# Kernel tuning notes

Hardware: AMD Instinct MI355X
Metric: run time of the kernel (lower is better)

## Reference

```python
import jax, jax.numpy as jnp
import numpy as np

N = 100_000          # nodes
E = 3_200_000        # edges (avg degree 32)
USER_SIZE = 80_000
CAT_SIZE = 5_000
USER_DIM = 8
CAT_DIM = 4
IN_CH = 8
OUT_CH = 16
HID = 16


def setup_inputs() -> dict:
    key = jax.random.key(0)
    ks = jax.random.split(key, 24)
    # features: [N,3] int; col0 = id (user id if type==0 else category id), col1 = known flag in {0,1}, col2 = type in {0,1}
    typ = jax.random.randint(ks[0], (N,), 0, 2)
    uid = jax.random.randint(ks[1], (N,), 0, USER_SIZE)
    cid = jax.random.randint(ks[2], (N,), 0, CAT_SIZE)
    col0 = jnp.where(typ == 0, uid, cid)
    col1 = jax.random.randint(ks[3], (N,), 0, 2)
    features = jnp.stack([col0, col1, typ], axis=1).astype(jnp.int64)
    edges = jax.random.randint(ks[4], (2, E), 0, N).astype(jnp.int64)

    def p(k, shape):
        return jax.random.normal(k, shape, dtype=jnp.float32) * 0.1

    return {
        "edges": edges,
        "features": features,
        "emb_user": p(ks[5], (USER_SIZE, USER_DIM)),
        "emb_known": p(ks[6], (2, USER_DIM)),
        "w_user": p(ks[7], (USER_DIM, IN_CH)),
        "b_user": p(ks[8], (IN_CH,)),
        "emb_cat": p(ks[9], (CAT_SIZE, CAT_DIM)),
        "w_cat": p(ks[10], (CAT_DIM, IN_CH)),
        "b_cat": p(ks[11], (IN_CH,)),
        "w0": p(ks[12], (IN_CH, HID)),
        "b0": p(ks[13], (HID,)),
        "w2": p(ks[14], (HID, OUT_CH)),
        "b2": p(ks[15], (OUT_CH,)),
        "w_node": p(ks[16], (OUT_CH, 2)),
        "b_node": p(ks[17], (2,)),
        "w_mem": p(ks[18], (OUT_CH, 1)),
        "b_mem": p(ks[19], (1,)),
    }


def _gcn_conv(x, w, b, src, dst, edge_norm, self_norm, n):
    h = x @ w                                      # [N, out]
    msgs = h[src] * edge_norm[:, None]             # [E, out] gather + scale
    agg = jax.ops.segment_sum(msgs, dst, num_segments=n)  # scatter-add
    agg = agg + h * self_norm[:, None]             # self-loop term
    return agg + b


def reference(edges, features, emb_user, emb_known, w_user, b_user, emb_cat,
              w_cat, b_cat, w0, b0, w2, b2, w_node, b_node, w_mem, b_mem):
    n = features.shape[0]
    typ = features[:, -1]
    is_user = (typ == 0)

    # --- input encoding (masked gather/scatter expressed as dense select) ---
    uidx = jnp.clip(features[:, 0], 0, emb_user.shape[0] - 1)
    kidx = jnp.clip(features[:, 1], 0, 1)
    cidx = jnp.clip(features[:, 0], 0, emb_cat.shape[0] - 1)
    user_f = jax.nn.relu(emb_user[uidx] + emb_known[kidx]) @ w_user + b_user
    cat_f = jax.nn.relu(emb_cat[cidx]) @ w_cat + b_cat
    x = jnp.where(is_user[:, None], user_f, cat_f)  # [N, IN_CH]

    # --- GCN normalization (shared across layers) ---
    src, dst = edges[0], edges[1]
    deg = jax.ops.segment_sum(jnp.ones((src.shape[0],), x.dtype), dst,
                              num_segments=n) + 1.0  # +1 for self-loop
    dinv = jax.lax.rsqrt(deg)
    edge_norm = dinv[src] * dinv[dst]
    self_norm = dinv * dinv

    # NOTE: original forward loop skips layers[1] entirely (enumerate over layers[:-2],
    # then applies layers[-1]); dropout branch (i>1) never triggers. Faithful here.
    h = jax.nn.relu(_gcn_conv(x, w0, b0, src, dst, edge_norm, self_norm, n))
    h = jax.nn.relu(_gcn_conv(h, w2, b2, src, dst, edge_norm, self_norm, n))

    member_pred = h @ w_mem + b_mem   # [N, 1]
    node_pred = h @ w_node + b_node   # [N, 2]
    return (member_pred, node_pred)
```

## Files before the change

### kernel.cpp

```cpp
#include <hip/hip_runtime.h>
#include <hip/hip_fp16.h>

#define BLK 256
#define PBLK 1024
#define NPB 256
#define CSHIFT 10
#define CNODES 1024
#define CMASK 1023
#define NBCMAX 128
#define CAP 40960
#define SSHIFT 6
#define NSL 16
#define SROWS 64
#define SRMASK 63
#define NCHK 8
#define FCAP2 384
#define FXS 1048576.0f
#define FXI (1.0f / 1048576.0f)

typedef int v4i __attribute__((ext_vector_type(4)));

static inline int cdiv(int a, int b) { return (a + b - 1) / b; }

__global__ void __launch_bounds__(PBLK)
k_hist(const int* __restrict__ dst, int* __restrict__ histG, int e, int nb) {
    __shared__ int h[NBCMAX];
    int tid = threadIdx.x;
    for (int t = tid; t < nb; t += PBLK) h[t] = 0;
    __syncthreads();
    int per = ((e + (int)gridDim.x - 1) / (int)gridDim.x + 3) & ~3;
    int beg = blockIdx.x * per;
    int end = min(e, beg + per);
    if (beg < end) {
        int m4 = beg + ((end - beg) & ~3);
        for (int i = beg + tid * 4; i < m4; i += PBLK * 4) {
            v4i d4 = __builtin_nontemporal_load((const v4i*)(dst + i));
            atomicAdd(&h[d4[0] >> CSHIFT], 1);
            atomicAdd(&h[d4[1] >> CSHIFT], 1);
            atomicAdd(&h[d4[2] >> CSHIFT], 1);
            atomicAdd(&h[d4[3] >> CSHIFT], 1);
        }
        int it = m4 + tid;
        if (it < end) atomicAdd(&h[dst[it] >> CSHIFT], 1);
    }
    __syncthreads();
    for (int t = tid; t < nb; t += PBLK) histG[(size_t)blockIdx.x * nb + t] = h[t];
}

__global__ void __launch_bounds__(NPB)
k_base(const int* __restrict__ histG, int* __restrict__ baseG, int* __restrict__ tot, int nb) {
    __shared__ int s[NPB];
    int b = blockIdx.x;
    int t = threadIdx.x;
    int hc = histG[(size_t)t * nb + b];
    int r = (hc + 15) & ~15;
    s[t] = r;
    __syncthreads();
    for (int off = 1; off < NPB; off <<= 1) {
        int v = (t >= off) ? s[t - off] : 0;
        __syncthreads();
        s[t] += v;
        __syncthreads();
    }
    int excl = s[t] - r;
    baseG[(size_t)t * nb + b] = b * CAP + excl;
    if (t == NPB - 1) tot[b] = min(s[t], CAP);
}

__global__ void __launch_bounds__(PBLK)
k_scatter(const int* __restrict__ src, const int* __restrict__ dst,
          const int* __restrict__ baseG, int* __restrict__ slab, int e, int nb) {
    __shared__ int cur[NBCMAX];
    int tid = threadIdx.x;
    int blk = blockIdx.x;
    for (int t = tid; t < nb; t += PBLK) cur[t] = baseG[(size_t)blk * nb + t];
    __syncthreads();
    int per = ((e + (int)gridDim.x - 1) / (int)gridDim.x + 3) & ~3;
    int beg = blk * per;
    int end = min(e, beg + per);
    if (beg < end) {
        int m4 = beg + ((end - beg) & ~3);
        for (int i = beg + tid * 4; i < m4; i += PBLK * 4) {
            v4i s4 = __builtin_nontemporal_load((const v4i*)(src + i));
            v4i d4 = __builtin_nontemporal_load((const v4i*)(dst + i));
#pragma unroll
            for (int k = 0; k < 4; ++k) {
                int d = d4[k];
                int b = d >> CSHIFT;
                int pos = atomicAdd(&cur[b], 1);
                if (pos < (b + 1) * CAP) slab[pos] = (s4[k] << CSHIFT) | (d & CMASK);
            }
        }
        int it = m4 + tid;
        if (it < end) {
            int d = dst[it];
            int b = d >> CSHIFT;
            int pos = atomicAdd(&cur[b], 1);
            if (pos < (b + 1) * CAP) slab[pos] = (src[it] << CSHIFT) | (d & CMASK);
        }
    }
    __syncthreads();
    for (int bb = tid; bb < nb; bb += PBLK) {
        int c = cur[bb];
        int lim = (bb + 1) * CAP;
        while ((c & 15) && c < lim) slab[c++] = -1;
    }
}

__global__ void __launch_bounds__(PBLK)
k_refine(const int* __restrict__ tot, const int* __restrict__ cslab,
         int* __restrict__ fslab, int* __restrict__ ftot,
         int* __restrict__ deg, int n) {
    __shared__ int cur[NSL];
    __shared__ int cnt[CNODES];
    int tid = threadIdx.x;
    int b = blockIdx.x >> 3;
    int p = blockIdx.x & 7;
    if (tid < NSL) cur[tid] = 0;
    for (int t = tid; t < CNODES; t += PBLK) cnt[t] = 0;
    __syncthreads();
    int nlines = tot[b] >> 4;
    int q0 = ((p * nlines) >> 3) << 2;
    int q1 = (((p + 1) * nlines) >> 3) << 2;
    const v4i* sl4 = reinterpret_cast<const v4i*>(cslab + (size_t)b * CAP);
    for (int i = q0 + tid; i < q1; i += PBLK) {
        v4i e4 = sl4[i];
#pragma unroll
        for (int k = 0; k < 4; ++k) {
            int e = e4[k];
            if (e >= 0) {
                int s = (e >> SSHIFT) & (NSL - 1);
                int fe = ((e >> CSHIFT) << SSHIFT) | (e & SRMASK);
                atomicAdd(&cnt[e & CMASK], 1);
                int pos = atomicAdd(&cur[s], 1);
                if (pos < FCAP2) fslab[(size_t)((b * NSL + s) * NCHK + p) * FCAP2 + pos] = fe;
            }
        }
    }
    __syncthreads();
    if (tid < NSL) {
        int cc = min(cur[tid], FCAP2);
        int r = min((cc + 15) & ~15, FCAP2);
        int* seg = fslab + (size_t)((b * NSL + tid) * NCHK + p) * FCAP2;
        for (int x = cc; x < r; ++x) seg[x] = -1;
        ftot[(b * NSL + tid) * NCHK + p] = r;
    }
    for (int t = tid; t < CNODES; t += PBLK) {
        int v = cnt[t];
        int nd = b * CNODES + t;
        if (v && nd < n) atomicAdd(&deg[nd], v);
    }
}

__global__ void k_featmm(const int* __restrict__ feat,
                         const float* __restrict__ emb_user,
                         const float* __restrict__ emb_known,
                         const float* __restrict__ w_user,
                         const float* __restrict__ b_user,
                         const float* __restrict__ emb_cat,
                         const float* __restrict__ w_cat,
                         const float* __restrict__ b_cat,
                         const float* __restrict__ w0,
                         const int* __restrict__ deg,
                         __half* __restrict__ Hs,
                         int n, int user_max, int cat_max) {
    __shared__ float w0s[8 * 16];
    for (int t = threadIdx.x; t < 8 * 16; t += blockDim.x) w0s[t] = w0[t];
    __syncthreads();
    int i = blockIdx.x * blockDim.x + threadIdx.x;
    if (i >= n) return;
    int col0 = feat[i * 3 + 0];
    int col1 = feat[i * 3 + 1];
    int typ  = feat[i * 3 + 2];
    float x[8];
    if (typ == 0) {
        int u = min(max(col0, 0), user_max);
        int k = min(max(col1, 0), 1);
        const float4* eu = reinterpret_cast<const float4*>(emb_user + (size_t)u * 8);
        const float4* ek = reinterpret_cast<const float4*>(emb_known + (size_t)k * 8);
        float4 a0 = eu[0], a1 = eu[1], k0 = ek[0], k1 = ek[1];
        float in[8];
        in[0] = fmaxf(a0.x + k0.x, 0.f); in[1] = fmaxf(a0.y + k0.y, 0.f);
        in[2] = fmaxf(a0.z + k0.z, 0.f); in[3] = fmaxf(a0.w + k0.w, 0.f);
        in[4] = fmaxf(a1.x + k1.x, 0.f); in[5] = fmaxf(a1.y + k1.y, 0.f);
        in[6] = fmaxf(a1.z + k1.z, 0.f); in[7] = fmaxf(a1.w + k1.w, 0.f);
#pragma unroll
        for (int c = 0; c < 8; ++c) {
            float s = b_user[c];
#pragma unroll
            for (int d = 0; d < 8; ++d) s += in[d] * w_user[d * 8 + c];
            x[c] = s;
        }
    } else {
        int ci = min(max(col0, 0), cat_max);
        float4 c0 = reinterpret_cast<const float4*>(emb_cat + (size_t)ci * 4)[0];
        float in[4];
        in[0] = fmaxf(c0.x, 0.f); in[1] = fmaxf(c0.y, 0.f);
        in[2] = fmaxf(c0.z, 0.f); in[3] = fmaxf(c0.w, 0.f);
#pragma unroll
        for (int c = 0; c < 8; ++c) {
            float s = b_cat[c];
#pragma unroll
            for (int d = 0; d < 4; ++d) s += in[d] * w_cat[d * 8 + c];
            x[c] = s;
        }
    }
    float dv = rsqrtf((float)deg[i] + 1.0f);
    float o[16];
#pragma unroll
    for (int c = 0; c < 16; ++c) {
        float s = 0.f;
#pragma unroll
        for (int d = 0; d < 8; ++d) s += x[d] * w0s[d * 16 + c];
        o[c] = s * dv;
    }
    union { __half2 h[8]; uint4 u[2]; } pk;
#pragma unroll
    for (int k = 0; k < 8; ++k) pk.h[k] = __floats2half2_rn(o[2 * k], o[2 * k + 1]);
    uint4* dp = reinterpret_cast<uint4*>(Hs + (size_t)i * 16);
    dp[0] = pk.u[0];
    dp[1] = pk.u[1];
}

__device__ __forceinline__ void gather_pair(const int* __restrict__ run0, int n0,
                                            const int* __restrict__ run1, int n1,
                                            const uint4* __restrict__ Hs4,
                                            int (*acc)[17], int tid) {
    const v4i* sl0 = reinterpret_cast<const v4i*>(run0);
    const v4i* sl1 = reinterpret_cast<const v4i*>(run1);
    int ns0 = n0 >> 2, ns1 = n1 >> 2;
    int maxs = max(ns0, ns1);
    int g = tid >> 1, q = tid & 1;
    for (int base = 0; base < maxs; base += 128) {
        int i = base + g;
        v4i e0 = sl0[min(i, (FCAP2 >> 2) - 1)];
        v4i e1 = sl1[min(i, (FCAP2 >> 2) - 1)];
        bool b0 = i < ns0, b1 = i < ns1;
        int us[8];
        us[0] = b0 ? e0[0] : -1; us[1] = b0 ? e0[1] : -1;
        us[2] = b0 ? e0[2] : -1; us[3] = b0 ? e0[3] : -1;
        us[4] = b1 ? e1[0] : -1; us[5] = b1 ? e1[1] : -1;
        us[6] = b1 ? e1[2] : -1; us[7] = b1 ? e1[3] : -1;
        uint4 v[8];
#pragma unroll
        for (int k = 0; k < 8; ++k)
            if (us[k] >= 0) v[k] = Hs4[(size_t)(us[k] >> SSHIFT) * 2 + q];
#pragma unroll
        for (int k = 0; k < 8; ++k) {
            if (us[k] >= 0) {
                int dl = us[k] & SRMASK;
                union { uint4 u4; __half2 h[4]; } c;
                c.u4 = v[k];
#pragma unroll
                for (int j = 0; j < 4; ++j) {
                    float2 f = __half22float2(c.h[j]);
                    atomicAdd(&acc[dl][8 * q + 2 * j + 0], __float2int_rn(f.x * FXS));
                    atomicAdd(&acc[dl][8 * q + 2 * j + 1], __float2int_rn(f.y * FXS));
                }
            }
        }
    }
}

__device__ __forceinline__ void gather_fb(const int* __restrict__ ftot,
                                          const int* __restrict__ fslab,
                                          int fb, const uint4* __restrict__ Hs4,
                                          int (*acc)[17], int tid) {
#pragma unroll
    for (int p = 0; p < NCHK; p += 2) {
        const int* r0 = fslab + (size_t)(fb * NCHK + p) * FCAP2;
        const int* r1 = fslab + (size_t)(fb * NCHK + p + 1) * FCAP2;
        gather_pair(r0, ftot[fb * NCHK + p], r1, ftot[fb * NCHK + p + 1], Hs4, acc, tid);
    }
}

__global__ void __launch_bounds__(BLK, 8)
k_bconv1(const int* __restrict__ ftot, const int* __restrict__ fslab,
         const __half* __restrict__ Hs, const int* __restrict__ deg,
         const float* __restrict__ b0, const float* __restrict__ w2,
         __half* __restrict__ Hs2, int n) {
    __shared__ int acc[SROWS][17];
    __shared__ float w2s[16 * 16];
    __shared__ float b0s[16];
    int tid = threadIdx.x;
    for (int t = tid; t < SROWS * 17; t += BLK) ((int*)acc)[t] = 0;
    w2s[tid] = w2[tid];
    if (tid < 16) b0s[tid] = b0[tid];
    __syncthreads();
    int fb = blockIdx.x;
    gather_fb(ftot, fslab, fb, reinterpret_cast<const uint4*>(Hs), acc, tid);
    __syncthreads();
    int nd = (fb >> 4) * CNODES + (fb & (NSL - 1)) * SROWS + tid;
    if (tid < SROWS && nd < n) {
        float dv = rsqrtf((float)deg[nd] + 1.0f);
        const __half* hrow = Hs + (size_t)nd * 16;
        float h1[16];
#pragma unroll
        for (int c = 0; c < 16; ++c) {
            float v = dv * ((float)acc[tid][c] * FXI + __half2float(hrow[c])) + b0s[c];
            h1[c] = v > 0.f ? v : 0.f;
        }
        float o[16];
#pragma unroll
        for (int c2 = 0; c2 < 16; ++c2) {
            float sum = 0.f;
#pragma unroll
            for (int c = 0; c < 16; ++c) sum += h1[c] * w2s[c * 16 + c2];
            o[c2] = sum * dv;
        }
        union { __half2 h[8]; uint4 u[2]; } pk;
#pragma unroll
        for (int k = 0; k < 8; ++k) pk.h[k] = __floats2half2_rn(o[2 * k], o[2 * k + 1]);
        uint4* dp = reinterpret_cast<uint4*>(Hs2 + (size_t)nd * 16);
        dp[0] = pk.u[0];
        dp[1] = pk.u[1];
    }
}

__global__ void __launch_bounds__(BLK, 8)
k_bconv2(const int* __restrict__ ftot, const int* __restrict__ fslab,
         const __half* __restrict__ Hs, const int* __restrict__ deg,
         const float* __restrict__ b2,
         const float* __restrict__ w_mem, const float* __restrict__ b_mem,
         const float* __restrict__ w_node, const float* __restrict__ b_node,
         float* __restrict__ out, int n) {
    __shared__ int acc[SROWS][17];
    __shared__ float wms[16], wn0[16], wn1[16], b2s[16];
    int tid = threadIdx.x;
    for (int t = tid; t < SROWS * 17; t += BLK) ((int*)acc)[t] = 0;
    if (tid < 16) {
        wms[tid] = w_mem[tid];
        wn0[tid] = w_node[tid * 2 + 0];
        wn1[tid] = w_node[tid * 2 + 1];
        b2s[tid] = b2[tid];
    }
    __syncthreads();
    int fb = blockIdx.x;
    gather_fb(ftot, fslab, fb, reinterpret_cast<const uint4*>(Hs), acc, tid);
    __syncthreads();
    int nd = (fb >> 4) * CNODES + (fb & (NSL - 1)) * SROWS + tid;
    if (tid < SROWS && nd < n) {
        float dv = rsqrtf((float)deg[nd] + 1.0f);
        const __half* hrow = Hs + (size_t)nd * 16;
        float mph = b_mem[0];
        float n0 = b_node[0];
        float n1 = b_node[1];
#pragma unroll
        for (int c = 0; c < 16; ++c) {
            float v = dv * ((float)acc[tid][c] * FXI + __half2float(hrow[c])) + b2s[c];
            float h = v > 0.f ? v : 0.f;
            mph += h * wms[c];
            n0  += h * wn0[c];
            n1  += h * wn1[c];
        }
        out[nd] = mph;
        out[n + 2 * nd + 0] = n0;
        out[n + 2 * nd + 1] = n1;
    }
}

extern "C" void kernel_launch(void* const* d_in, const int* in_sizes, int n_in,
                              void* d_out, int out_size, void* d_ws, size_t ws_size,
                              hipStream_t stream) {
    const int*   edges     = (const int*)d_in[0];
    const int*   feat      = (const int*)d_in[1];
    const float* emb_user  = (const float*)d_in[2];
    const float* emb_known = (const float*)d_in[3];
    const float* w_user    = (const float*)d_in[4];
    const float* b_user    = (const float*)d_in[5];
    const float* emb_cat   = (const float*)d_in[6];
    const float* w_cat     = (const float*)d_in[7];
    const float* b_cat     = (const float*)d_in[8];
    const float* w0        = (const float*)d_in[9];
    const float* b0        = (const float*)d_in[10];
    const float* w2        = (const float*)d_in[11];
    const float* b2        = (const float*)d_in[12];
    const float* w_node    = (const float*)d_in[13];
    const float* b_node    = (const float*)d_in[14];
    const float* w_mem     = (const float*)d_in[15];
    const float* b_mem     = (const float*)d_in[16];

    const int E = in_sizes[0] / 2;
    const int n = in_sizes[1] / 3;
    const int user_max = in_sizes[2] / 8 - 1;
    const int cat_max  = in_sizes[6] / 4 - 1;
    const int NBC = cdiv(n, CNODES);
    const int NBF = NBC * NSL;

    const int* src = edges;
    const int* dst = edges + E;

    int* cslab   = (int*)d_ws;
    int* fslab   = cslab + (size_t)NBC * CAP;
    __half* hsA  = (__half*)(fslab + (size_t)NBF * NCHK * FCAP2);
    __half* hsB  = hsA + (size_t)n * 16;
    int* histG   = (int*)(hsB + (size_t)n * 16);
    int* baseG   = histG + (size_t)NPB * NBC;
    int* tot     = baseG + (size_t)NPB * NBC;
    int* deg     = tot + NBC;
    int* ftot    = deg + n;

    float* outp = (float*)d_out;

    hipMemsetAsync(deg, 0, (size_t)n * sizeof(int), stream);
    k_hist<<<NPB, PBLK, 0, stream>>>(dst, histG, E, NBC);
    k_base<<<NBC, NPB, 0, stream>>>(histG, baseG, tot, NBC);
    k_scatter<<<NPB, PBLK, 0, stream>>>(src, dst, baseG, cslab, E, NBC);
    k_refine<<<NBC * NCHK, PBLK, 0, stream>>>(tot, cslab, fslab, ftot, deg, n);
    k_featmm<<<cdiv(n, BLK), BLK, 0, stream>>>(feat, emb_user, emb_known, w_user, b_user,
                                               emb_cat, w_cat, b_cat, w0, deg, hsA,
                                               n, user_max, cat_max);
    k_bconv1<<<NBF, BLK, 0, stream>>>(ftot, fslab, hsA, deg, b0, w2, hsB, n);
    k_bconv2<<<NBF, BLK, 0, stream>>>(ftot, fslab, hsB, deg, b2,
                                      w_mem, b_mem, w_node, b_node, outp, n);
}
```

Before: 109.2 us.

## Pack two fixed-point channels per 64-bit LDS atomic and replicate histogram bins

The per-edge LDS accumulation now packs two biased 32-bit fixed-point channels into one 64-bit atomicAdd, which halves the number of shared-memory atomics in both conv gathers. The bias is removed afterward using the node degree. The histogram kernel keeps four wavefront-group replicas of its bins to cut atomic contention on a small set of counters. The conv1 epilogue also spreads the 16x16 matvec across all 256 threads, each computing 4 outputs, instead of only 64 threads. The packing depends on each biased lane never carrying into its neighbour, which limits the per-node degree and value range that stay correct.

```diff
diff --git a/kernel.cpp b/kernel.cpp
--- a/kernel.cpp
+++ b/kernel.cpp
@@ -17,16 +17,19 @@
 #define FCAP2 384
 #define FXS 1048576.0f
 #define FXI (1.0f / 1048576.0f)
+#define PBIAS (1 << 23)
 
 typedef int v4i __attribute__((ext_vector_type(4)));
+typedef unsigned long long u64;
 
 static inline int cdiv(int a, int b) { return (a + b - 1) / b; }
 
 __global__ void __launch_bounds__(PBLK)
 k_hist(const int* __restrict__ dst, int* __restrict__ histG, int e, int nb) {
-    __shared__ int h[NBCMAX];
+    __shared__ int h[4][NBCMAX];
     int tid = threadIdx.x;
-    for (int t = tid; t < nb; t += PBLK) h[t] = 0;
+    int rep = (tid >> 6) & 3;
+    for (int t = tid; t < 4 * NBCMAX; t += PBLK) ((int*)h)[t] = 0;
     __syncthreads();
     int per = ((e + (int)gridDim.x - 1) / (int)gridDim.x + 3) & ~3;
     int beg = blockIdx.x * per;
@@ -35,16 +38,17 @@
         int m4 = beg + ((end - beg) & ~3);
         for (int i = beg + tid * 4; i < m4; i += PBLK * 4) {
             v4i d4 = __builtin_nontemporal_load((const v4i*)(dst + i));
-            atomicAdd(&h[d4[0] >> CSHIFT], 1);
-            atomicAdd(&h[d4[1] >> CSHIFT], 1);
-            atomicAdd(&h[d4[2] >> CSHIFT], 1);
-            atomicAdd(&h[d4[3] >> CSHIFT], 1);
+            atomicAdd(&h[rep][d4[0] >> CSHIFT], 1);
+            atomicAdd(&h[rep][d4[1] >> CSHIFT], 1);
+            atomicAdd(&h[rep][d4[2] >> CSHIFT], 1);
+            atomicAdd(&h[rep][d4[3] >> CSHIFT], 1);
         }
         int it = m4 + tid;
-        if (it < end) atomicAdd(&h[dst[it] >> CSHIFT], 1);
-    }
-    __syncthreads();
-    for (int t = tid; t < nb; t += PBLK) histG[(size_t)blockIdx.x * nb + t] = h[t];
+        if (it < end) atomicAdd(&h[rep][dst[it] >> CSHIFT], 1);
+    }
+    __syncthreads();
+    for (int t = tid; t < nb; t += PBLK)
+        histG[(size_t)blockIdx.x * nb + t] = h[0][t] + h[1][t] + h[2][t] + h[3][t];
 }
 
 __global__ void __launch_bounds__(NPB)
@@ -225,7 +229,7 @@
 __device__ __forceinline__ void gather_pair(const int* __restrict__ run0, int n0,
                                             const int* __restrict__ run1, int n1,
                                             const uint4* __restrict__ Hs4,
-                                            int (*acc)[17], int tid) {
+                                            u64 (*acc64)[9], int tid) {
     const v4i* sl0 = reinterpret_cast<const v4i*>(run0);
     const v4i* sl1 = reinterpret_cast<const v4i*>(run1);
     int ns0 = n0 >> 2, ns1 = n1 >> 2;
@@ -254,8 +258,10 @@
 #pragma unroll
                 for (int j = 0; j < 4; ++j) {
                     float2 f = __half22float2(c.h[j]);
-                    atomicAdd(&acc[dl][8 * q + 2 * j + 0], __float2int_rn(f.x * FXS));
-                    atomicAdd(&acc[dl][8 * q + 2 * j + 1], __float2int_rn(f.y * FXS));
+                    unsigned a0 = (unsigned)(__float2int_rn(f.x * FXS) + PBIAS);
+                    unsigned a1 = (unsigned)(__float2int_rn(f.y * FXS) + PBIAS);
+                    u64 pk = ((u64)a1 << 32) | (u64)a0;
+                    atomicAdd(&acc64[dl][q * 4 + j], pk);
                 }
             }
         }
@@ -265,13 +271,20 @@
 __device__ __forceinline__ void gather_fb(const int* __restrict__ ftot,
                                           const int* __restrict__ fslab,
                                           int fb, const uint4* __restrict__ Hs4,
-                                          int (*acc)[17], int tid) {
+                                          u64 (*acc64)[9], int tid) {
 #pragma unroll
     for (int p = 0; p < NCHK; p += 2) {
         const int* r0 = fslab + (size_t)(fb * NCHK + p) * FCAP2;
         const int* r1 = fslab + (size_t)(fb * NCHK + p + 1) * FCAP2;
-        gather_pair(r0, ftot[fb * NCHK + p], r1, ftot[fb * NCHK + p + 1], Hs4, acc, tid);
-    }
+        gather_pair(r0, ftot[fb * NCHK + p], r1, ftot[fb * NCHK + p + 1], Hs4, acc64, tid);
+    }
+}
+
+__device__ __forceinline__ float unpack_acc(const u64 (*acc64)[9], int node, int c, int dg) {
+    u64 w = acc64[node][c >> 1];
+    unsigned raw = (c & 1) ? (unsigned)(w >> 32) : (unsigned)(w & 0xffffffffULL);
+    long long t = (long long)raw - (long long)dg * PBIAS;
+    return (float)t * FXI;
 }
 
 __global__ void __launch_bounds__(BLK, 8)
@@ -279,41 +292,42 @@
          const __half* __restrict__ Hs, const int* __restrict__ deg,
          const float* __restrict__ b0, const float* __restrict__ w2,
          __half* __restrict__ Hs2, int n) {
-    __shared__ int acc[SROWS][17];
+    __shared__ u64 acc64[SROWS][9];
     __shared__ float w2s[16 * 16];
     __shared__ float b0s[16];
     int tid = threadIdx.x;
-    for (int t = tid; t < SROWS * 17; t += BLK) ((int*)acc)[t] = 0;
+    for (int t = tid; t < SROWS * 9; t += BLK) ((u64*)acc64)[t] = 0ull;
     w2s[tid] = w2[tid];
     if (tid < 16) b0s[tid] = b0[tid];
     __syncthreads();
     int fb = blockIdx.x;
-    gather_fb(ftot, fslab, fb, reinterpret_cast<const uint4*>(Hs), acc, tid);
-    __syncthreads();
-    int nd = (fb >> 4) * CNODES + (fb & (NSL - 1)) * SROWS + tid;
-    if (tid < SROWS && nd < n) {
-        float dv = rsqrtf((float)deg[nd] + 1.0f);
+    gather_fb(ftot, fslab, fb, reinterpret_cast<const uint4*>(Hs), acc64, tid);
+    __syncthreads();
+    int node = tid & 63;
+    int qq = tid >> 6;
+    int nd = (fb >> 4) * CNODES + (fb & (NSL - 1)) * SROWS + node;
+    if (nd < n) {
+        int dg = deg[nd];
+        float dv = rsqrtf((float)dg + 1.0f);
         const __half* hrow = Hs + (size_t)nd * 16;
         float h1[16];
 #pragma unroll
         for (int c = 0; c < 16; ++c) {
-            float v = dv * ((float)acc[tid][c] * FXI + __half2float(hrow[c])) + b0s[c];
+            float v = dv * (unpack_acc(acc64, node, c, dg) + __half2float(hrow[c])) + b0s[c];
             h1[c] = v > 0.f ? v : 0.f;
         }
-        float o[16];
-#pragma unroll
-        for (int c2 = 0; c2 < 16; ++c2) {
+        float o[4];
+#pragma unroll
+        for (int j = 0; j < 4; ++j) {
             float sum = 0.f;
 #pragma unroll
-            for (int c = 0; c < 16; ++c) sum += h1[c] * w2s[c * 16 + c2];
-            o[c2] = sum * dv;
-        }
-        union { __half2 h[8]; uint4 u[2]; } pk;
-#pragma unroll
-        for (int k = 0; k < 8; ++k) pk.h[k] = __floats2half2_rn(o[2 * k], o[2 * k + 1]);
-        uint4* dp = reinterpret_cast<uint4*>(Hs2 + (size_t)nd * 16);
-        dp[0] = pk.u[0];
-        dp[1] = pk.u[1];
+            for (int c = 0; c < 16; ++c) sum += h1[c] * w2s[c * 16 + qq * 4 + j];
+            o[j] = sum * dv;
+        }
+        union { __half2 h[2]; uint2 u; } pk;
+        pk.h[0] = __floats2half2_rn(o[0], o[1]);
+        pk.h[1] = __floats2half2_rn(o[2], o[3]);
+        *reinterpret_cast<uint2*>(Hs2 + (size_t)nd * 16 + qq * 4) = pk.u;
     }
 }
 
@@ -324,10 +338,10 @@
          const float* __restrict__ w_mem, const float* __restrict__ b_mem,
          const float* __restrict__ w_node, const float* __restrict__ b_node,
          float* __restrict__ out, int n) {
-    __shared__ int acc[SROWS][17];
+    __shared__ u64 acc64[SROWS][9];
     __shared__ float wms[16], wn0[16], wn1[16], b2s[16];
     int tid = threadIdx.x;
-    for (int t = tid; t < SROWS * 17; t += BLK) ((int*)acc)[t] = 0;
+    for (int t = tid; t < SROWS * 9; t += BLK) ((u64*)acc64)[t] = 0ull;
     if (tid < 16) {
         wms[tid] = w_mem[tid];
         wn0[tid] = w_node[tid * 2 + 0];
@@ -336,18 +350,19 @@
     }
     __syncthreads();
     int fb = blockIdx.x;
-    gather_fb(ftot, fslab, fb, reinterpret_cast<const uint4*>(Hs), acc, tid);
+    gather_fb(ftot, fslab, fb, reinterpret_cast<const uint4*>(Hs), acc64, tid);
     __syncthreads();
     int nd = (fb >> 4) * CNODES + (fb & (NSL - 1)) * SROWS + tid;
     if (tid < SROWS && nd < n) {
-        float dv = rsqrtf((float)deg[nd] + 1.0f);
+        int dg = deg[nd];
+        float dv = rsqrtf((float)dg + 1.0f);
         const __half* hrow = Hs + (size_t)nd * 16;
         float mph = b_mem[0];
         float n0 = b_node[0];
         float n1 = b_node[1];
 #pragma unroll
         for (int c = 0; c < 16; ++c) {
-            float v = dv * ((float)acc[tid][c] * FXI + __half2float(hrow[c])) + b2s[c];
+            float v = dv * (unpack_acc(acc64, tid, c, dg) + __half2float(hrow[c])) + b2s[c];
             float h = v > 0.f ? v : 0.f;
             mph += h * wms[c];
             n0  += h * wn0[c];
```

Result: no change. 108.4 us (-0.7%).
